# Kernel tuning notes

Hardware: AMD Instinct MI355X
Metric: run time of the kernel (lower is better)

Reference implementation:

```python
import jax, jax.numpy as jnp
import numpy as np

N_NODES = 50000
N_EDGES = 800000
N_GRAPHS = 512
VOCAB = 100000
EMB = 64
HID = 128
CLASSES = 2


def setup_inputs() -> dict:
    key = jax.random.key(0)
    ks = jax.random.split(key, 12)
    x = jax.random.randint(ks[0], (N_NODES,), 0, VOCAB)
    edge_index = jax.random.randint(ks[1], (2, N_EDGES), 0, N_NODES)
    batch = jnp.sort(jax.random.randint(ks[2], (N_NODES,), 0, N_GRAPHS))
    s = lambda fan_in: 1.0 / np.sqrt(fan_in)
    emb_table = jax.random.normal(ks[3], (VOCAB, EMB), jnp.float32)
    w1_l = jax.random.uniform(ks[4], (EMB, HID), jnp.float32, -s(EMB), s(EMB))
    b1 = jnp.zeros((HID,), jnp.float32)
    w1_r = jax.random.uniform(ks[5], (EMB, HID), jnp.float32, -s(EMB), s(EMB))
    w2_l = jax.random.uniform(ks[6], (HID, HID), jnp.float32, -s(HID), s(HID))
    b2 = jnp.zeros((HID,), jnp.float32)
    w2_r = jax.random.uniform(ks[7], (HID, HID), jnp.float32, -s(HID), s(HID))
    w_out = jax.random.uniform(ks[8], (HID, CLASSES), jnp.float32, -s(HID), s(HID))
    b_out = jnp.zeros((CLASSES,), jnp.float32)
    return {"x": x, "edge_index": edge_index, "batch": batch,
            "emb_table": emb_table, "w1_l": w1_l, "b1": b1, "w1_r": w1_r,
            "w2_l": w2_l, "b2": b2, "w2_r": w2_r, "w_out": w_out, "b_out": b_out}


def _sage_conv(h, src, dst, w_l, b_l, w_r):
    # PyG SAGEConv (mean aggr): out = lin_l(mean_{j in N(i)} x_j) + lin_r(x_i)
    msg = h[src]                                              # [E, F] gather
    agg = jax.ops.segment_sum(msg, dst, num_segments=N_NODES)  # [N, F]
    deg = jax.ops.segment_sum(jnp.ones((src.shape[0],), h.dtype), dst,
                              num_segments=N_NODES)
    mean = agg / jnp.maximum(deg, 1.0)[:, None]
    return mean @ w_l + b_l + h @ w_r


def reference(x, edge_index, batch, emb_table, w1_l, b1, w1_r,
              w2_l, b2, w2_r, w_out, b_out):
    src, dst = edge_index[0], edge_index[1]
    h = emb_table[x]                                          # [N, EMB]
    h = jax.nn.relu(_sage_conv(h, src, dst, w1_l, b1, w1_r))
    # dropout is identity in eval mode
    h = jax.nn.relu(_sage_conv(h, src, dst, w2_l, b2, w2_r))
    # global mean pool over graphs
    pooled = jax.ops.segment_sum(h, batch, num_segments=N_GRAPHS)
    cnt = jax.ops.segment_sum(jnp.ones((N_NODES,), h.dtype), batch,
                              num_segments=N_GRAPHS)
    pooled = pooled / jnp.maximum(cnt, 1.0)[:, None]
    return pooled @ w_out + b_out                              # [G, CLASSES]
```

## Files before the change

kernel.cpp:

```cpp
#include <hip/hip_runtime.h>
#include <hip/hip_bf16.h>

#define N_NODES 50000
#define N_EDGES 800000
#define N_GRAPHS 512
#define EMB 64
#define HID 128

__global__ void k_embed_hist(const int* __restrict__ x, const float* __restrict__ emb,
                             const int* __restrict__ ei, float* __restrict__ h0,
                             int* __restrict__ deg) {
    int t = blockIdx.x * 256 + threadIdx.x;
    if (t >= N_EDGES) return;
    int n = t >> 4, c4 = t & 15;
    const float4* e4 = (const float4*)emb;
    ((float4*)h0)[(size_t)n * 16 + c4] = e4[(size_t)x[n] * 16 + c4];
    atomicAdd(&deg[ei[N_EDGES + t]], 1);
}

__global__ void k_scanA(const int* __restrict__ deg, int* __restrict__ rowptr,
                        int* __restrict__ bsums) {
    __shared__ int s[256];
    int t = threadIdx.x, i = blockIdx.x * 256 + t;
    int v = (i < N_NODES) ? deg[i] : 0;
    s[t] = v; __syncthreads();
    int xv = v;
    for (int off = 1; off < 256; off <<= 1) {
        int y = (t >= off) ? s[t - off] : 0;
        __syncthreads();
        xv += y; s[t] = xv;
        __syncthreads();
    }
    if (i < N_NODES) rowptr[i] = xv - v;
    if (t == 255) bsums[blockIdx.x] = xv;
}

__global__ void k_scanB(int* __restrict__ bsums, int nb) {
    __shared__ int s[256];
    int t = threadIdx.x;
    int v = (t < nb) ? bsums[t] : 0;
    s[t] = v; __syncthreads();
    int xv = v;
    for (int off = 1; off < 256; off <<= 1) {
        int y = (t >= off) ? s[t - off] : 0;
        __syncthreads();
        xv += y; s[t] = xv;
        __syncthreads();
    }
    if (t < nb) bsums[t] = xv - v;
}

__global__ void k_scanC(int* __restrict__ rowptr, int* __restrict__ wp,
                        const int* __restrict__ bsums) {
    int i = blockIdx.x * 256 + threadIdx.x;
    if (i < N_NODES) {
        int v = rowptr[i] + bsums[blockIdx.x];
        rowptr[i] = v;
        wp[i] = v;
    }
    if (i == 0) rowptr[N_NODES] = N_EDGES;
}

__global__ void k_scatter(const int* __restrict__ ei, int* __restrict__ wp,
                          int* __restrict__ nbr) {
    int e = blockIdx.x * 256 + threadIdx.x;
    if (e >= N_EDGES) return;
    int s = ei[e], d = ei[N_EDGES + e];
    int pos = atomicAdd(&wp[d], 1);
    nbr[pos] = s;
}

template <int F>
__global__ __launch_bounds__(256) void k_agg(const float* __restrict__ h,
                                             const int* __restrict__ rowptr,
                                             const int* __restrict__ nbr,
                                             float* __restrict__ mean) {
    int wid = (blockIdx.x * 256 + threadIdx.x) >> 6;
    int lane = threadIdx.x & 63;
    if (wid >= N_NODES) return;
    int r0 = rowptr[wid], r1 = rowptr[wid + 1];
    float inv = 1.0f / (float)max(r1 - r0, 1);
    if constexpr (F == 64) {
        float a0 = 0.f, a1 = 0.f, a2 = 0.f, a3 = 0.f;
        int i = r0;
        for (; i + 3 < r1; i += 4) {
            int s0 = nbr[i], s1 = nbr[i + 1], s2 = nbr[i + 2], s3 = nbr[i + 3];
            a0 += h[(size_t)s0 * 64 + lane];
            a1 += h[(size_t)s1 * 64 + lane];
            a2 += h[(size_t)s2 * 64 + lane];
            a3 += h[(size_t)s3 * 64 + lane];
        }
        for (; i < r1; ++i) a0 += h[(size_t)nbr[i] * 64 + lane];
        mean[(size_t)wid * 64 + lane] = ((a0 + a1) + (a2 + a3)) * inv;
    } else {
        const float2* h2 = (const float2*)h;
        float2 a0 = {0.f, 0.f}, a1 = {0.f, 0.f}, a2 = {0.f, 0.f}, a3 = {0.f, 0.f};
        int i = r0;
        for (; i + 3 < r1; i += 4) {
            int s0 = nbr[i], s1 = nbr[i + 1], s2 = nbr[i + 2], s3 = nbr[i + 3];
            float2 v0 = h2[(size_t)s0 * 64 + lane];
            float2 v1 = h2[(size_t)s1 * 64 + lane];
            float2 v2 = h2[(size_t)s2 * 64 + lane];
            float2 v3 = h2[(size_t)s3 * 64 + lane];
            a0.x += v0.x; a0.y += v0.y;
            a1.x += v1.x; a1.y += v1.y;
            a2.x += v2.x; a2.y += v2.y;
            a3.x += v3.x; a3.y += v3.y;
        }
        for (; i < r1; ++i) {
            float2 v = h2[(size_t)nbr[i] * 64 + lane];
            a0.x += v.x; a0.y += v.y;
        }
        float2* m2 = (float2*)mean;
        m2[(size_t)wid * 64 + lane] =
            make_float2(((a0.x + a1.x) + (a2.x + a3.x)) * inv,
                        ((a0.y + a1.y) + (a2.y + a3.y)) * inv);
    }
}

template <int K>
__global__ __launch_bounds__(256) void k_layer(
    const float* __restrict__ hself, const float* __restrict__ hmean,
    const float* __restrict__ w_r, const float* __restrict__ w_l,
    const float* __restrict__ bias, float* __restrict__ out) {
    constexpr int LS = K + 2;
    __shared__ float ls[64 * LS];
    int base = blockIdx.x * 64;
    int t = threadIdx.x;
    int lane = t & 63;
    int wid = __builtin_amdgcn_readfirstlane(t >> 6);
    int j0 = wid * 32;
    int node = base + lane;
    bool valid = node < N_NODES;

    float acc[32];
    #pragma unroll
    for (int j = 0; j < 32; j++) acc[j] = bias[j0 + j];

    const float* lrow = &ls[lane * LS];
    const float4* h4;

    h4 = (const float4*)hself;
    for (int idx = t; idx < 64 * (K / 4); idx += 256) {
        int r = idx / (K / 4), c4 = idx % (K / 4);
        float4 v = (base + r < N_NODES) ? h4[(size_t)(base + r) * (K / 4) + c4]
                                        : make_float4(0.f, 0.f, 0.f, 0.f);
        float* dp = &ls[r * LS + c4 * 4];
        dp[0] = v.x; dp[1] = v.y; dp[2] = v.z; dp[3] = v.w;
    }
    __syncthreads();
    #pragma unroll 4
    for (int k = 0; k < K; k++) {
        float hv = lrow[k];
        const float* wk = &w_r[(size_t)k * 128 + j0];
        #pragma unroll
        for (int j = 0; j < 32; j++) acc[j] = fmaf(hv, wk[j], acc[j]);
    }
    __syncthreads();

    h4 = (const float4*)hmean;
    for (int idx = t; idx < 64 * (K / 4); idx += 256) {
        int r = idx / (K / 4), c4 = idx % (K / 4);
        float4 v = (base + r < N_NODES) ? h4[(size_t)(base + r) * (K / 4) + c4]
                                        : make_float4(0.f, 0.f, 0.f, 0.f);
        float* dp = &ls[r * LS + c4 * 4];
        dp[0] = v.x; dp[1] = v.y; dp[2] = v.z; dp[3] = v.w;
    }
    __syncthreads();
    #pragma unroll 4
    for (int k = 0; k < K; k++) {
        float hv = lrow[k];
        const float* wk = &w_l[(size_t)k * 128 + j0];
        #pragma unroll
        for (int j = 0; j < 32; j++) acc[j] = fmaf(hv, wk[j], acc[j]);
    }

    if (!valid) return;
    float4* o4 = (float4*)out;
    #pragma unroll
    for (int jj = 0; jj < 8; jj++) {
        float4 v;
        v.x = fmaxf(acc[jj * 4 + 0], 0.f);
        v.y = fmaxf(acc[jj * 4 + 1], 0.f);
        v.z = fmaxf(acc[jj * 4 + 2], 0.f);
        v.w = fmaxf(acc[jj * 4 + 3], 0.f);
        o4[(size_t)node * 32 + (j0 >> 2) + jj] = v;
    }
}

__global__ void k_pool_head(const float* __restrict__ h2, const int* __restrict__ batch,
                            const float* __restrict__ w_out, const float* __restrict__ b_out,
                            float* __restrict__ out) {
    int g = blockIdx.x;
    int lo = 0, hi = N_NODES;
    while (lo < hi) { int mid = (lo + hi) >> 1; if (batch[mid] < g) lo = mid + 1; else hi = mid; }
    int s = lo;
    lo = s; hi = N_NODES;
    while (lo < hi) { int mid = (lo + hi) >> 1; if (batch[mid] < g + 1) lo = mid + 1; else hi = mid; }
    int e = lo;

    int f = threadIdx.x & 127, half = threadIdx.x >> 7;
    float acc = 0.0f;
    for (int r = s + half; r < e; r += 2) acc += h2[(size_t)r * 128 + f];
    __shared__ float tmp[256];
    tmp[threadIdx.x] = acc;
    __syncthreads();
    if (half == 0) {
        float p = (tmp[f] + tmp[f + 128]) / (float)max(e - s, 1);
        tmp[f]       = p * w_out[f * 2 + 0];
        tmp[f + 128] = p * w_out[f * 2 + 1];
    }
    __syncthreads();
    for (int str = 64; str > 0; str >>= 1) {
        if (threadIdx.x < str) {
            tmp[threadIdx.x] += tmp[threadIdx.x + str];
            tmp[threadIdx.x + 128] += tmp[threadIdx.x + 128 + str];
        }
        __syncthreads();
    }
    if (threadIdx.x == 0) {
        out[(size_t)g * 2 + 0] = tmp[0] + b_out[0];
        out[(size_t)g * 2 + 1] = tmp[128] + b_out[1];
    }
}

extern "C" void kernel_launch(void* const* d_in, const int* in_sizes, int n_in,
                              void* d_out, int out_size, void* d_ws, size_t ws_size,
                              hipStream_t stream) {
    const int*   x      = (const int*)d_in[0];
    const int*   ei     = (const int*)d_in[1];
    const int*   batch  = (const int*)d_in[2];
    const float* emb    = (const float*)d_in[3];
    const float* w1_l   = (const float*)d_in[4];
    const float* b1     = (const float*)d_in[5];
    const float* w1_r   = (const float*)d_in[6];
    const float* w2_l   = (const float*)d_in[7];
    const float* b2     = (const float*)d_in[8];
    const float* w2_r   = (const float*)d_in[9];
    const float* w_out  = (const float*)d_in[10];
    const float* b_out  = (const float*)d_in[11];
    float* out = (float*)d_out;

    float* F = (float*)d_ws;
    float* h0    = F;
    float* mean1 = h0 + (size_t)N_NODES * 64;
    float* h1    = mean1 + (size_t)N_NODES * 64;
    float* mean2 = h1 + (size_t)N_NODES * 128;
    float* h2    = h0;
    int*   deg   = (int*)(mean2 + (size_t)N_NODES * 128);
    int*   rowptr= deg + N_NODES;
    int*   wp    = rowptr + N_NODES + 1;
    int*   nbr   = wp + N_NODES;
    int*   bsums = nbr + N_EDGES;

    const int NB = (N_NODES + 255) / 256;

    hipMemsetAsync(deg, 0, (size_t)N_NODES * sizeof(int), stream);

    k_embed_hist<<<(N_EDGES + 255) / 256, 256, 0, stream>>>(x, emb, ei, h0, deg);
    k_scanA<<<NB, 256, 0, stream>>>(deg, rowptr, bsums);
    k_scanB<<<1, 256, 0, stream>>>(bsums, NB);
    k_scanC<<<NB, 256, 0, stream>>>(rowptr, wp, bsums);
    k_scatter<<<(N_EDGES + 255) / 256, 256, 0, stream>>>(ei, wp, nbr);

    k_agg<64><<<(N_NODES + 3) / 4, 256, 0, stream>>>(h0, rowptr, nbr, mean1);
    k_layer<64><<<(N_NODES + 63) / 64, 256, 0, stream>>>(h0, mean1, w1_r, w1_l, b1, h1);

    k_agg<128><<<(N_NODES + 3) / 4, 256, 0, stream>>>(h1, rowptr, nbr, mean2);
    k_layer<128><<<(N_NODES + 63) / 64, 256, 0, stream>>>(h1, mean2, w2_r, w2_l, b2, h2);

    k_pool_head<<<N_GRAPHS, 256, 0, stream>>>(h2, batch, w_out, b_out, out);

    (void)in_sizes; (void)n_in; (void)out_size; (void)ws_size;
}
```

Before: 387.7 us.

## Pack multiple nodes per wavefront in aggregation and widen layer blocks to 512 threads

The neighbor aggregation kernel now assigns 4 nodes (F=64) or 2 nodes (F=128) per wavefront, and each lane does float4 gathers instead of scalar or float2 loads. This gives more independent memory requests in flight and fewer idle lanes. The dense layer kernel goes from 256 to 512 threads, with each wave computing 16 output columns instead of 32. That halves per-thread accumulator registers and raises occupancy, and the LDS row padding changes from K+2 to K+1. In exchange, each block makes more redundant LDS reads of the node rows, and the divergence between nodes that share a wave grows with degree variance.

```diff
diff --git a/kernel.cpp b/kernel.cpp
--- a/kernel.cpp
+++ b/kernel.cpp
@@ -75,78 +75,75 @@
                                              const int* __restrict__ rowptr,
                                              const int* __restrict__ nbr,
                                              float* __restrict__ mean) {
-    int wid = (blockIdx.x * 256 + threadIdx.x) >> 6;
-    int lane = threadIdx.x & 63;
-    if (wid >= N_NODES) return;
-    int r0 = rowptr[wid], r1 = rowptr[wid + 1];
+    int w = (blockIdx.x * 256 + threadIdx.x) >> 6;
+    int l = threadIdx.x & 63;
+    const float4* h4 = (const float4*)h;
+    float4* m4 = (float4*)mean;
+
+    int n, c;
+    if constexpr (F == 128) { n = w * 2 + (l >> 5); c = l & 31; }
+    else                    { n = w * 4 + (l >> 4); c = l & 15; }
+    if (n >= N_NODES) return;
+    constexpr int C = F / 4;
+
+    int r0 = rowptr[n], r1 = rowptr[n + 1];
     float inv = 1.0f / (float)max(r1 - r0, 1);
-    if constexpr (F == 64) {
-        float a0 = 0.f, a1 = 0.f, a2 = 0.f, a3 = 0.f;
-        int i = r0;
-        for (; i + 3 < r1; i += 4) {
-            int s0 = nbr[i], s1 = nbr[i + 1], s2 = nbr[i + 2], s3 = nbr[i + 3];
-            a0 += h[(size_t)s0 * 64 + lane];
-            a1 += h[(size_t)s1 * 64 + lane];
-            a2 += h[(size_t)s2 * 64 + lane];
-            a3 += h[(size_t)s3 * 64 + lane];
-        }
-        for (; i < r1; ++i) a0 += h[(size_t)nbr[i] * 64 + lane];
-        mean[(size_t)wid * 64 + lane] = ((a0 + a1) + (a2 + a3)) * inv;
-    } else {
-        const float2* h2 = (const float2*)h;
-        float2 a0 = {0.f, 0.f}, a1 = {0.f, 0.f}, a2 = {0.f, 0.f}, a3 = {0.f, 0.f};
-        int i = r0;
-        for (; i + 3 < r1; i += 4) {
-            int s0 = nbr[i], s1 = nbr[i + 1], s2 = nbr[i + 2], s3 = nbr[i + 3];
-            float2 v0 = h2[(size_t)s0 * 64 + lane];
-            float2 v1 = h2[(size_t)s1 * 64 + lane];
-            float2 v2 = h2[(size_t)s2 * 64 + lane];
-            float2 v3 = h2[(size_t)s3 * 64 + lane];
-            a0.x += v0.x; a0.y += v0.y;
-            a1.x += v1.x; a1.y += v1.y;
-            a2.x += v2.x; a2.y += v2.y;
-            a3.x += v3.x; a3.y += v3.y;
-        }
-        for (; i < r1; ++i) {
-            float2 v = h2[(size_t)nbr[i] * 64 + lane];
-            a0.x += v.x; a0.y += v.y;
-        }
-        float2* m2 = (float2*)mean;
-        m2[(size_t)wid * 64 + lane] =
-            make_float2(((a0.x + a1.x) + (a2.x + a3.x)) * inv,
-                        ((a0.y + a1.y) + (a2.y + a3.y)) * inv);
-    }
+
+    float4 a0 = {0,0,0,0}, a1 = {0,0,0,0}, a2 = {0,0,0,0}, a3 = {0,0,0,0};
+    int i = r0;
+    for (; i + 3 < r1; i += 4) {
+        int s0 = nbr[i], s1 = nbr[i + 1], s2 = nbr[i + 2], s3 = nbr[i + 3];
+        float4 v0 = h4[(size_t)s0 * C + c];
+        float4 v1 = h4[(size_t)s1 * C + c];
+        float4 v2 = h4[(size_t)s2 * C + c];
+        float4 v3 = h4[(size_t)s3 * C + c];
+        a0.x += v0.x; a0.y += v0.y; a0.z += v0.z; a0.w += v0.w;
+        a1.x += v1.x; a1.y += v1.y; a1.z += v1.z; a1.w += v1.w;
+        a2.x += v2.x; a2.y += v2.y; a2.z += v2.z; a2.w += v2.w;
+        a3.x += v3.x; a3.y += v3.y; a3.z += v3.z; a3.w += v3.w;
+    }
+    for (; i < r1; ++i) {
+        float4 v = h4[(size_t)nbr[i] * C + c];
+        a0.x += v.x; a0.y += v.y; a0.z += v.z; a0.w += v.w;
+    }
+    float4 r;
+    r.x = ((a0.x + a1.x) + (a2.x + a3.x)) * inv;
+    r.y = ((a0.y + a1.y) + (a2.y + a3.y)) * inv;
+    r.z = ((a0.z + a1.z) + (a2.z + a3.z)) * inv;
+    r.w = ((a0.w + a1.w) + (a2.w + a3.w)) * inv;
+    m4[(size_t)n * C + c] = r;
 }
 
 template <int K>
-__global__ __launch_bounds__(256) void k_layer(
+__global__ __launch_bounds__(512) void k_layer(
     const float* __restrict__ hself, const float* __restrict__ hmean,
     const float* __restrict__ w_r, const float* __restrict__ w_l,
     const float* __restrict__ bias, float* __restrict__ out) {
-    constexpr int LS = K + 2;
+    constexpr int LS = K + 1;
     __shared__ float ls[64 * LS];
     int base = blockIdx.x * 64;
     int t = threadIdx.x;
     int lane = t & 63;
     int wid = __builtin_amdgcn_readfirstlane(t >> 6);
-    int j0 = wid * 32;
+    int j0 = wid * 16;
     int node = base + lane;
     bool valid = node < N_NODES;
 
-    float acc[32];
+    float acc[16];
     #pragma unroll
-    for (int j = 0; j < 32; j++) acc[j] = bias[j0 + j];
+    for (int j = 0; j < 16; j++) acc[j] = bias[j0 + j];
 
     const float* lrow = &ls[lane * LS];
-    const float4* h4;
-
-    h4 = (const float4*)hself;
-    for (int idx = t; idx < 64 * (K / 4); idx += 256) {
-        int r = idx / (K / 4), c4 = idx % (K / 4);
-        float4 v = (base + r < N_NODES) ? h4[(size_t)(base + r) * (K / 4) + c4]
-                                        : make_float4(0.f, 0.f, 0.f, 0.f);
-        float* dp = &ls[r * LS + c4 * 4];
-        dp[0] = v.x; dp[1] = v.y; dp[2] = v.z; dp[3] = v.w;
+
+    {
+        const float4* h4 = (const float4*)hself;
+        for (int idx = t; idx < 64 * (K / 4); idx += 512) {
+            int r = idx / (K / 4), c4 = idx % (K / 4);
+            float4 v = (base + r < N_NODES) ? h4[(size_t)(base + r) * (K / 4) + c4]
+                                            : make_float4(0.f, 0.f, 0.f, 0.f);
+            float* dp = &ls[r * LS + c4 * 4];
+            dp[0] = v.x; dp[1] = v.y; dp[2] = v.z; dp[3] = v.w;
+        }
     }
     __syncthreads();
     #pragma unroll 4
@@ -154,17 +151,19 @@
         float hv = lrow[k];
         const float* wk = &w_r[(size_t)k * 128 + j0];
         #pragma unroll
-        for (int j = 0; j < 32; j++) acc[j] = fmaf(hv, wk[j], acc[j]);
-    }
-    __syncthreads();
-
-    h4 = (const float4*)hmean;
-    for (int idx = t; idx < 64 * (K / 4); idx += 256) {
-        int r = idx / (K / 4), c4 = idx % (K / 4);
-        float4 v = (base + r < N_NODES) ? h4[(size_t)(base + r) * (K / 4) + c4]
-                                        : make_float4(0.f, 0.f, 0.f, 0.f);
-        float* dp = &ls[r * LS + c4 * 4];
-        dp[0] = v.x; dp[1] = v.y; dp[2] = v.z; dp[3] = v.w;
+        for (int j = 0; j < 16; j++) acc[j] = fmaf(hv, wk[j], acc[j]);
+    }
+    __syncthreads();
+
+    {
+        const float4* h4 = (const float4*)hmean;
+        for (int idx = t; idx < 64 * (K / 4); idx += 512) {
+            int r = idx / (K / 4), c4 = idx % (K / 4);
+            float4 v = (base + r < N_NODES) ? h4[(size_t)(base + r) * (K / 4) + c4]
+                                            : make_float4(0.f, 0.f, 0.f, 0.f);
+            float* dp = &ls[r * LS + c4 * 4];
+            dp[0] = v.x; dp[1] = v.y; dp[2] = v.z; dp[3] = v.w;
+        }
     }
     __syncthreads();
     #pragma unroll 4
@@ -172,19 +171,19 @@
         float hv = lrow[k];
         const float* wk = &w_l[(size_t)k * 128 + j0];
         #pragma unroll
-        for (int j = 0; j < 32; j++) acc[j] = fmaf(hv, wk[j], acc[j]);
+        for (int j = 0; j < 16; j++) acc[j] = fmaf(hv, wk[j], acc[j]);
     }
 
     if (!valid) return;
     float4* o4 = (float4*)out;
     #pragma unroll
-    for (int jj = 0; jj < 8; jj++) {
+    for (int jj = 0; jj < 4; jj++) {
         float4 v;
         v.x = fmaxf(acc[jj * 4 + 0], 0.f);
         v.y = fmaxf(acc[jj * 4 + 1], 0.f);
         v.z = fmaxf(acc[jj * 4 + 2], 0.f);
         v.w = fmaxf(acc[jj * 4 + 3], 0.f);
-        o4[(size_t)node * 32 + (j0 >> 2) + jj] = v;
+        o4[(size_t)node * 32 + wid * 4 + jj] = v;
     }
 }
 
@@ -263,11 +262,11 @@
     k_scanC<<<NB, 256, 0, stream>>>(rowptr, wp, bsums);
     k_scatter<<<(N_EDGES + 255) / 256, 256, 0, stream>>>(ei, wp, nbr);
 
-    k_agg<64><<<(N_NODES + 3) / 4, 256, 0, stream>>>(h0, rowptr, nbr, mean1);
-    k_layer<64><<<(N_NODES + 63) / 64, 256, 0, stream>>>(h0, mean1, w1_r, w1_l, b1, h1);
-
-    k_agg<128><<<(N_NODES + 3) / 4, 256, 0, stream>>>(h1, rowptr, nbr, mean2);
-    k_layer<128><<<(N_NODES + 63) / 64, 256, 0, stream>>>(h1, mean2, w2_r, w2_l, b2, h2);
+    k_agg<64><<<(N_NODES + 15) / 16, 256, 0, stream>>>(h0, rowptr, nbr, mean1);
+    k_layer<64><<<(N_NODES + 63) / 64, 512, 0, stream>>>(h0, mean1, w1_r, w1_l, b1, h1);
+
+    k_agg<128><<<(N_NODES + 7) / 8, 256, 0, stream>>>(h1, rowptr, nbr, mean2);
+    k_layer<128><<<(N_NODES + 63) / 64, 512, 0, stream>>>(h1, mean2, w2_r, w2_l, b2, h2);
 
     k_pool_head<<<N_GRAPHS, 256, 0, stream>>>(h2, batch, w_out, b_out, out);
 
```

Result: no change. 387.3 us (-0.1%).
